# Optimization experiments

Hardware: AMD Instinct MI355X
Metric: run time of the kernel (lower is better)

The kernel has to match this reference:

```python
import jax, jax.numpy as jnp
import numpy as np

B, H, W = 2, 64, 1024
C1, C2 = 64, 128
MLP = [128, 128]
KH, KW = 5, 5
NS = 3
DIST = 100.0
BN_EPS = 1e-5


def setup_inputs() -> dict:
    key = jax.random.key(0)
    ks = jax.random.split(key, 12)
    inp = {
        "xyz1_proj": jax.random.normal(ks[0], (B, H, W, 3), jnp.float32),
        "xyz2_proj": jax.random.normal(ks[1], (B, H, W, 3), jnp.float32),
        "feat1_proj": jax.random.normal(ks[2], (B, H, W, C1), jnp.float32),
        "feat2_proj": jax.random.normal(ks[3], (B, H, W, C2), jnp.float32),
    }
    cin = C1 + C2
    chans = [cin] + MLP
    for i in range(len(MLP)):
        inp[f"w{i}"] = jax.random.normal(ks[4 + 2 * i], (chans[i], chans[i + 1]), jnp.float32) * 0.05
        inp[f"b{i}"] = jnp.zeros((chans[i + 1],), jnp.float32)
        inp[f"g{i}"] = jnp.ones((chans[i + 1],), jnp.float32)
        inp[f"be{i}"] = jnp.zeros((chans[i + 1],), jnp.float32)
    return inp


def _grid_knn(xyz1, xyz2):
    """Structured-grid KNN (no_sort_knn): for each query pixel, scan a KHxKW
    window in row-major order and take the first NS in-bounds neighbors whose
    squared distance is below DIST^2. Returns flat neighbor indices (B,N,NS)
    and a validity mask (B,N,NS,1)."""
    b, h, w, _ = xyz1.shape
    n = h * w
    k = KH * KW
    x1 = xyz1.reshape(b, n, 3)
    x2 = xyz2.reshape(b, n, 3)
    oh = jnp.repeat(jnp.arange(KH) - KH // 2, KW)   # (K,)
    ow = jnp.tile(jnp.arange(KW) - KW // 2, KH)     # (K,)
    nh = jnp.arange(h)[:, None, None] + oh[None, None, :]   # (H,1,K)
    nw = jnp.arange(w)[None, :, None] + ow[None, None, :]   # (1,W,K)
    inb = ((nh >= 0) & (nh < h)) & ((nw >= 0) & (nw < w))    # (H,W,K)
    flat = jnp.clip(nh, 0, h - 1) * w + jnp.clip(nw, 0, w - 1)
    flat = jnp.broadcast_to(flat, (h, w, k)).reshape(n, k)
    inb = jnp.broadcast_to(inb, (h, w, k)).reshape(n, k)
    # window gather: (B,N,K,3)
    neigh = jnp.take(x2, flat.reshape(-1), axis=1).reshape(b, n, k, 3)
    sq = jnp.sum(jnp.square(neigh - x1[:, :, None, :]), -1)  # (B,N,K)
    valid = inb[None] & (sq < DIST * DIST)
    v = valid.astype(jnp.int32)
    rank = jnp.cumsum(v, -1) - v  # rank among valid, scan order
    sel, fnd = [], []
    for j in range(NS):
        hit = valid & (rank == j)
        sel.append(jnp.argmax(hit, -1))
        fnd.append(jnp.any(hit, -1))
    sel = jnp.stack(sel, -1)          # (B,N,NS) window slot
    found = jnp.stack(fnd, -1)        # (B,N,NS)
    flat_b = jnp.broadcast_to(flat[None], (b, n, k))
    sel_flat = jnp.take_along_axis(flat_b, sel, axis=-1)
    sel_flat = jnp.where(found, sel_flat, 0)  # zeros like the init buffers
    mask = found.astype(x1.dtype)[..., None]  # (B,N,NS,1)
    return sel_flat, mask


def _gather(feat_flat, sel_flat):
    # feat_flat: (B,N,C), sel_flat: (B,N,NS) -> (B,N,NS,C)
    b, n, c = feat_flat.shape
    idx = sel_flat.reshape(b, n * NS, 1)
    g = jnp.take_along_axis(feat_flat, jnp.broadcast_to(idx, (b, n * NS, c)), axis=1)
    return g.reshape(b, n, NS, c)


def reference(xyz1_proj, xyz2_proj, feat1_proj, feat2_proj,
              w0, b0, g0, be0, w1, b1, g1, be1):
    b, h, w, _ = xyz1_proj.shape
    n = h * w
    xyz1 = xyz1_proj.reshape(b, n, 3)
    xyz2 = xyz2_proj.reshape(b, n, 3)
    feat2 = feat2_proj.reshape(b, n, -1)

    sel_flat, mask = _grid_knn(xyz1_proj, xyz2_proj)
    mask = jax.lax.stop_gradient(mask)

    grouped_xyz = _gather(xyz2, sel_flat) * mask          # (B,N,NS,3)
    grouped_feat = _gather(feat2, sel_flat) * mask        # (B,N,NS,C2)

    dist = jnp.sum(jnp.square(grouped_xyz - xyz1[:, :, None, :]), -1)  # (B,N,NS)
    dist = jnp.where(dist < 1e-10, jnp.full_like(dist, 1e-10), dist)
    norm = jnp.sum(1.0 / dist, axis=2, keepdims=True)     # (B,N,1)
    weight = (1.0 / dist) / norm                          # (B,N,NS)
    interp = jnp.sum(grouped_feat * weight[..., None], axis=2)  # (B,N,C2)

    x = jnp.concatenate([feat1_proj.reshape(b, n, -1), interp], -1)  # (B,N,C1+C2)

    # 1x1 conv MLP with training-mode BatchNorm + ReLU
    for (wi, bi, gi, bei) in ((w0, b0, g0, be0), (w1, b1, g1, be1)):
        x = x @ wi + bi
        mu = jnp.mean(x, axis=(0, 1))
        var = jnp.var(x, axis=(0, 1))
        x = (x - mu) * jax.lax.rsqrt(var + BN_EPS) * gi + bei
        x = jax.nn.relu(x)
    return x  # (B, H*W, MLP[-1])
```

## Files before the change

### kernel.cpp

```cpp
#include <hip/hip_runtime.h>

#define H_    64
#define W_    1024
#define NPT   65536
#define NTOT  131072
#define C1_   64
#define C2_   128
#define CIN_  192
#define CM_   128
#define NS_   3
#define DIST2_ 10000.0f
#define BN_EPS_ 1e-5f
#define NSLOT 32
#define XP    132

typedef __attribute__((ext_vector_type(8))) short short8;
typedef __attribute__((ext_vector_type(4))) float floatx4;

static __device__ __forceinline__ unsigned short f2bf(float f) {
    unsigned int u = __float_as_uint(f);
    u += 0x7fffu + ((u >> 16) & 1u);
    return (unsigned short)(u >> 16);
}
static __device__ __forceinline__ float bflo(unsigned u) { return __uint_as_float(u << 16); }
static __device__ __forceinline__ float bfhi(unsigned u) { return __uint_as_float(u & 0xffff0000u); }
static __device__ __forceinline__ unsigned packbf(float a, float b) {
    return (unsigned)f2bf(a) | ((unsigned)f2bf(b) << 16);
}

__global__ __launch_bounds__(256) void prep_w_kernel(
    const float* __restrict__ w0, const float* __restrict__ w1,
    unsigned short* __restrict__ w0F, unsigned short* __restrict__ w1F)
{
    int tid = blockIdx.x * 256 + threadIdx.x;
    if (tid < 3072) {
        int c = tid, lane = c & 63, nt = (c >> 6) & 7, kk = c >> 9;
        int n = nt * 16 + (lane & 15);
        int kb = kk * 32 + (lane >> 4) * 8;
        #pragma unroll
        for (int j = 0; j < 8; j++)
            w0F[(size_t)c * 8 + j] = f2bf(w0[(size_t)(kb + j) * CM_ + n]);
    } else if (tid < 5120) {
        int c = tid - 3072, lane = c & 63, nt = (c >> 6) & 7, kk = c >> 9;
        int n = nt * 16 + (lane & 15);
        int kb = kk * 32 + (lane >> 4) * 8;
        #pragma unroll
        for (int j = 0; j < 8; j++)
            w1F[(size_t)c * 8 + j] = f2bf(w1[(size_t)(kb + j) * CM_ + n]);
    }
}

static __device__ __forceinline__ void bn_finish_lds(
    const float* __restrict__ slots, const float* __restrict__ g,
    const float* __restrict__ be, float* bnpL, int t)
{
    if (t < CM_) {
        float s = 0.f, q2 = 0.f;
        #pragma unroll
        for (int sl = 0; sl < NSLOT; sl++) {
            s  += slots[sl * 256 + t];
            q2 += slots[sl * 256 + CM_ + t];
        }
        const float invn = 1.0f / (float)NTOT;
        float mu = s * invn, var = q2 * invn - mu * mu;
        float sc = g[t] * rsqrtf(var + BN_EPS_);
        bnpL[t] = sc;
        bnpL[CM_ + t] = be[t] - mu * sc;
    }
}

__global__ __launch_bounds__(256, 2) void fused1_kernel(
    const float* __restrict__ xyz1, const float* __restrict__ xyz2,
    const float* __restrict__ feat1, const float* __restrict__ feat2,
    const unsigned short* __restrict__ w0F, const float* __restrict__ b0,
    uint4* __restrict__ y0w4, float* __restrict__ slots0)
{
    __shared__ __align__(16) char smem[64 * XP * 2];
    __shared__ int   selL[64][NS_];
    __shared__ float wgtL[64][NS_];
    __shared__ float wsum[4][CM_], wsq[4][CM_];

    float (*sqL)[28] = (float (*)[28])smem;
    unsigned short (*xstage)[XP] = (unsigned short (*)[XP])smem;

    const int t = threadIdx.x;
    const int blk = blockIdx.x;
    const int pbase = blk * 64;
    const int bidx = blk >> 10;
    const int wv = t >> 6, lane = t & 63;
    const int m = lane & 15, q = lane >> 4;
    const int lr = wv * 16 + m;
    const int row0 = pbase + lr;

    short8 af[2];
    #pragma unroll
    for (int kk = 0; kk < 2; kk++) {
        const float* sp = feat1 + (size_t)row0 * C1_ + kk * 32 + q * 8;
        float4 fa = *(const float4*)(sp), fb = *(const float4*)(sp + 4);
        short8 a;
        a[0] = f2bf(fa.x); a[1] = f2bf(fa.y); a[2] = f2bf(fa.z); a[3] = f2bf(fa.w);
        a[4] = f2bf(fb.x); a[5] = f2bf(fb.y); a[6] = f2bf(fb.z); a[7] = f2bf(fb.w);
        af[kk] = a;
    }

    {
        const int p = t >> 2, g = t & 3;
        const int pt = pbase + p;
        const int n = pt & (NPT - 1);
        const int h = n >> 10, w = n & (W_ - 1);
        const float* p1 = xyz1 + (size_t)pt * 3;
        float x1 = p1[0], y1 = p1[1], z1 = p1[2];
        const float* x2b = xyz2 + (size_t)bidx * NPT * 3;
        #pragma unroll
        for (int j = 0; j < 7; j++) {
            int k = g * 7 + j;
            if (k < 25) {
                int dh = k / 5 - 2, dw = k % 5 - 2;
                int nh = h + dh, nw = w + dw;
                bool inb = (nh >= 0) && (nh < H_) && (nw >= 0) && (nw < W_);
                int ch = min(max(nh, 0), H_ - 1);
                int cw = min(max(nw, 0), W_ - 1);
                const float* p2 = x2b + (size_t)(ch * W_ + cw) * 3;
                float dx = p2[0] - x1, dy = p2[1] - y1, dz = p2[2] - z1;
                sqL[p][k] = inb ? (dx * dx + dy * dy + dz * dz) : 3.4e38f;
            }
        }
    }
    __syncthreads();

    if (t < 64) {
        const int pt = pbase + t;
        const int n = pt & (NPT - 1);
        const int h = n >> 10, w = n & (W_ - 1);
        const float* p1 = xyz1 + (size_t)pt * 3;
        float x1 = p1[0], y1 = p1[1], z1 = p1[2];

        int   s0 = 0, s1 = 0, s2 = 0;
        float d0 = 0.f, d1 = 0.f, d2 = 0.f;
        int cnt = 0;
        #pragma unroll
        for (int k = 0; k < 25; k++) {
            const int dh = k / 5 - 2, dw = k % 5 - 2;
            int ch = min(max(h + dh, 0), H_ - 1);
            int cw = min(max(w + dw, 0), W_ - 1);
            int nidx = ch * W_ + cw;
            float sk = sqL[t][k];
            if (sk < DIST2_ && cnt < NS_) {
                if (cnt == 0)      { s0 = nidx; d0 = sk; }
                else if (cnt == 1) { s1 = nidx; d1 = sk; }
                else               { s2 = nidx; d2 = sk; }
                cnt++;
            }
        }
        float self2 = x1 * x1 + y1 * y1 + z1 * z1;
        float dd0 = (cnt > 0) ? d0 : self2;
        float dd1 = (cnt > 1) ? d1 : self2;
        float dd2 = (cnt > 2) ? d2 : self2;
        dd0 = fmaxf(dd0, 1e-10f); dd1 = fmaxf(dd1, 1e-10f); dd2 = fmaxf(dd2, 1e-10f);
        float i0 = 1.0f / dd0, i1 = 1.0f / dd1, i2 = 1.0f / dd2;
        float norm = i0 + i1 + i2;
        selL[t][0] = (cnt > 0) ? s0 : 0;
        selL[t][1] = (cnt > 1) ? s1 : 0;
        selL[t][2] = (cnt > 2) ? s2 : 0;
        wgtL[t][0] = (cnt > 0) ? i0 / norm : 0.f;
        wgtL[t][1] = (cnt > 1) ? i1 / norm : 0.f;
        wgtL[t][2] = (cnt > 2) ? i2 / norm : 0.f;
    }
    __syncthreads();

    const float* f2b = feat2 + (size_t)bidx * NPT * C2_;
    #pragma unroll
    for (int i = 0; i < 8; i++) {
        int idx = t + i * 256;
        int p = idx >> 5, c4 = (idx & 31) << 2;
        float ax = 0.f, ay = 0.f, az = 0.f, aw = 0.f;
        #pragma unroll
        for (int j = 0; j < NS_; j++) {
            float wj = wgtL[p][j];
            const float4 f = *(const float4*)(f2b + (size_t)selL[p][j] * C2_ + c4);
            ax += wj * f.x; ay += wj * f.y; az += wj * f.z; aw += wj * f.w;
        }
        ushort4 u;
        u.x = f2bf(ax); u.y = f2bf(ay); u.z = f2bf(az); u.w = f2bf(aw);
        *(ushort4*)&xstage[p][c4] = u;
    }
    __syncthreads();

    floatx4 acc[8];
    #pragma unroll
    for (int nt = 0; nt < 8; nt++) acc[nt] = (floatx4){0.f, 0.f, 0.f, 0.f};

    #pragma unroll
    for (int kk = 0; kk < 6; kk++) {
        short8 bw[8];
        #pragma unroll
        for (int nt = 0; nt < 8; nt++)
            bw[nt] = *(const short8*)(w0F + ((size_t)(kk * 8 + nt) * 64 + lane) * 8);
        short8 a = (kk < 2) ? af[kk]
                            : *(const short8*)&xstage[lr][(kk - 2) * 32 + q * 8];
        #pragma unroll
        for (int nt = 0; nt < 8; nt++)
            acc[nt] = __builtin_amdgcn_mfma_f32_16x16x32_bf16(a, bw[nt], acc[nt], 0, 0, 0);
    }

    #pragma unroll
    for (int nt2 = 0; nt2 < 4; nt2++) {
        const int ntA = 2 * nt2, ntB = ntA + 1;
        const int nA = ntA * 16 + m, nB = ntB * 16 + m;
        float bvA = b0[nA], bvB = b0[nB];
        unsigned u0 = packbf(acc[ntA][0] + bvA, acc[ntA][1] + bvA);
        unsigned u1 = packbf(acc[ntA][2] + bvA, acc[ntA][3] + bvA);
        unsigned u2 = packbf(acc[ntB][0] + bvB, acc[ntB][1] + bvB);
        unsigned u3 = packbf(acc[ntB][2] + bvB, acc[ntB][3] + bvB);
        y0w4[((size_t)(blk * 4 + wv) * 4 + nt2) * 64 + lane] = make_uint4(u0, u1, u2, u3);
        float a0 = bflo(u0), a1 = bfhi(u0), a2 = bflo(u1), a3 = bfhi(u1);
        float b0v = bflo(u2), b1v = bfhi(u2), b2v = bflo(u3), b3v = bfhi(u3);
        float sA = a0 + a1 + a2 + a3, qA = a0*a0 + a1*a1 + a2*a2 + a3*a3;
        float sB = b0v + b1v + b2v + b3v, qB = b0v*b0v + b1v*b1v + b2v*b2v + b3v*b3v;
        sA += __shfl_xor(sA, 16, 64); qA += __shfl_xor(qA, 16, 64);
        sA += __shfl_xor(sA, 32, 64); qA += __shfl_xor(qA, 32, 64);
        sB += __shfl_xor(sB, 16, 64); qB += __shfl_xor(qB, 16, 64);
        sB += __shfl_xor(sB, 32, 64); qB += __shfl_xor(qB, 32, 64);
        if (q == 0) {
            wsum[wv][nA] = sA; wsq[wv][nA] = qA;
            wsum[wv][nB] = sB; wsq[wv][nB] = qB;
        }
    }
    __syncthreads();

    float* slot = slots0 + (size_t)(blk & (NSLOT - 1)) * 256;
    if (t < CM_)
        atomicAdd(&slot[t], wsum[0][t] + wsum[1][t] + wsum[2][t] + wsum[3][t]);
    else
        atomicAdd(&slot[t], wsq[0][t - CM_] + wsq[1][t - CM_] + wsq[2][t - CM_] + wsq[3][t - CM_]);
}

__global__ __launch_bounds__(256, 2) void fused2_kernel(
    const uint4* __restrict__ y0w4, const float* __restrict__ slots0,
    const float* __restrict__ g0, const float* __restrict__ be0,
    const unsigned short* __restrict__ w1F, const float* __restrict__ b1,
    uint4* __restrict__ y1w4, float* __restrict__ slots1)
{
    __shared__ unsigned short x1s[64][XP];
    __shared__ float wsum[4][CM_], wsq[4][CM_];
    __shared__ float bnpL[2 * CM_];

    const int t = threadIdx.x;
    const int blk = blockIdx.x;
    const int wv = t >> 6, lane = t & 63;
    const int m = lane & 15, q = lane >> 4;
    const int lr = wv * 16 + m;

    short8 bw0[8];
    #pragma unroll
    for (int nt = 0; nt < 8; nt++)
        bw0[nt] = *(const short8*)(w1F + ((size_t)nt * 64 + lane) * 8);

    bn_finish_lds(slots0, g0, be0, bnpL, t);
    __syncthreads();

    #pragma unroll
    for (int nt2 = 0; nt2 < 4; nt2++) {
        const int nA = (2 * nt2) * 16 + m, nB = nA + 16;
        float scA = bnpL[nA], shA = bnpL[CM_ + nA];
        float scB = bnpL[nB], shB = bnpL[CM_ + nB];
        uint4 u = y0w4[((size_t)(blk * 4 + wv) * 4 + nt2) * 64 + lane];
        int rb = wv * 16 + q * 4;
        x1s[rb + 0][nA] = f2bf(fmaxf(bflo(u.x) * scA + shA, 0.f));
        x1s[rb + 1][nA] = f2bf(fmaxf(bfhi(u.x) * scA + shA, 0.f));
        x1s[rb + 2][nA] = f2bf(fmaxf(bflo(u.y) * scA + shA, 0.f));
        x1s[rb + 3][nA] = f2bf(fmaxf(bfhi(u.y) * scA + shA, 0.f));
        x1s[rb + 0][nB] = f2bf(fmaxf(bflo(u.z) * scB + shB, 0.f));
        x1s[rb + 1][nB] = f2bf(fmaxf(bfhi(u.z) * scB + shB, 0.f));
        x1s[rb + 2][nB] = f2bf(fmaxf(bflo(u.w) * scB + shB, 0.f));
        x1s[rb + 3][nB] = f2bf(fmaxf(bfhi(u.w) * scB + shB, 0.f));
    }
    __syncthreads();

    floatx4 acc[8];
    #pragma unroll
    for (int nt = 0; nt < 8; nt++) acc[nt] = (floatx4){0.f, 0.f, 0.f, 0.f};

    #pragma unroll
    for (int kk = 0; kk < 4; kk++) {
        short8 bw[8];
        #pragma unroll
        for (int nt = 0; nt < 8; nt++)
            bw[nt] = (kk == 0) ? bw0[nt]
                   : *(const short8*)(w1F + ((size_t)(kk * 8 + nt) * 64 + lane) * 8);
        short8 a = *(const short8*)&x1s[lr][kk * 32 + q * 8];
        #pragma unroll
        for (int nt = 0; nt < 8; nt++)
            acc[nt] = __builtin_amdgcn_mfma_f32_16x16x32_bf16(a, bw[nt], acc[nt], 0, 0, 0);
    }

    #pragma unroll
    for (int nt2 = 0; nt2 < 4; nt2++) {
        const int ntA = 2 * nt2, ntB = ntA + 1;
        const int nA = ntA * 16 + m, nB = ntB * 16 + m;
        float bvA = b1[nA], bvB = b1[nB];
        unsigned u0 = packbf(acc[ntA][0] + bvA, acc[ntA][1] + bvA);
        unsigned u1 = packbf(acc[ntA][2] + bvA, acc[ntA][3] + bvA);
        unsigned u2 = packbf(acc[ntB][0] + bvB, acc[ntB][1] + bvB);
        unsigned u3 = packbf(acc[ntB][2] + bvB, acc[ntB][3] + bvB);
        y1w4[((size_t)(blk * 4 + wv) * 4 + nt2) * 64 + lane] = make_uint4(u0, u1, u2, u3);
        float a0 = bflo(u0), a1 = bfhi(u0), a2 = bflo(u1), a3 = bfhi(u1);
        float c0 = bflo(u2), c1 = bfhi(u2), c2 = bflo(u3), c3 = bfhi(u3);
        float sA = a0 + a1 + a2 + a3, qA = a0*a0 + a1*a1 + a2*a2 + a3*a3;
        float sB = c0 + c1 + c2 + c3, qB = c0*c0 + c1*c1 + c2*c2 + c3*c3;
        sA += __shfl_xor(sA, 16, 64); qA += __shfl_xor(qA, 16, 64);
        sA += __shfl_xor(sA, 32, 64); qA += __shfl_xor(qA, 32, 64);
        sB += __shfl_xor(sB, 16, 64); qB += __shfl_xor(qB, 16, 64);
        sB += __shfl_xor(sB, 32, 64); qB += __shfl_xor(qB, 32, 64);
        if (q == 0) {
            wsum[wv][nA] = sA; wsq[wv][nA] = qA;
            wsum[wv][nB] = sB; wsq[wv][nB] = qB;
        }
    }
    __syncthreads();

    float* slot = slots1 + (size_t)(blk & (NSLOT - 1)) * 256;
    if (t < CM_)
        atomicAdd(&slot[t], wsum[0][t] + wsum[1][t] + wsum[2][t] + wsum[3][t]);
    else
        atomicAdd(&slot[t], wsq[0][t - CM_] + wsq[1][t - CM_] + wsq[2][t - CM_] + wsq[3][t - CM_]);
}

__global__ __launch_bounds__(256) void bn_out_kernel(
    const uint4* __restrict__ y1w4, const float* __restrict__ slots1,
    const float* __restrict__ g1, const float* __restrict__ be1,
    float* __restrict__ out)
{
    __shared__ float xo[64][XP];
    __shared__ float bnpL[2 * CM_];
    const int t = threadIdx.x;
    const int blk = blockIdx.x;
    const int wv = t >> 6, lane = t & 63;
    const int m = lane & 15, q = lane >> 4;

    bn_finish_lds(slots1, g1, be1, bnpL, t);
    __syncthreads();

    #pragma unroll
    for (int nt2 = 0; nt2 < 4; nt2++) {
        const int nA = (2 * nt2) * 16 + m, nB = nA + 16;
        float scA = bnpL[nA], shA = bnpL[CM_ + nA];
        float scB = bnpL[nB], shB = bnpL[CM_ + nB];
        uint4 u = y1w4[((size_t)(blk * 4 + wv) * 4 + nt2) * 64 + lane];
        int rb = wv * 16 + q * 4;
        xo[rb + 0][nA] = fmaxf(bflo(u.x) * scA + shA, 0.f);
        xo[rb + 1][nA] = fmaxf(bfhi(u.x) * scA + shA, 0.f);
        xo[rb + 2][nA] = fmaxf(bflo(u.y) * scA + shA, 0.f);
        xo[rb + 3][nA] = fmaxf(bfhi(u.y) * scA + shA, 0.f);
        xo[rb + 0][nB] = fmaxf(bflo(u.z) * scB + shB, 0.f);
        xo[rb + 1][nB] = fmaxf(bfhi(u.z) * scB + shB, 0.f);
        xo[rb + 2][nB] = fmaxf(bflo(u.w) * scB + shB, 0.f);
        xo[rb + 3][nB] = fmaxf(bfhi(u.w) * scB + shB, 0.f);
    }
    __syncthreads();

    const int pbase = blk * 64;
    #pragma unroll
    for (int i = 0; i < 8; i++) {
        int idx = t + i * 256;
        int p = idx >> 5, c4 = (idx & 31) << 2;
        float4 v = *(const float4*)&xo[p][c4];
        *(float4*)(out + (size_t)(pbase + p) * CM_ + c4) = v;
    }
}

extern "C" void kernel_launch(void* const* d_in, const int* in_sizes, int n_in,
                              void* d_out, int out_size, void* d_ws, size_t ws_size,
                              hipStream_t stream)
{
    const float* xyz1  = (const float*)d_in[0];
    const float* xyz2  = (const float*)d_in[1];
    const float* feat1 = (const float*)d_in[2];
    const float* feat2 = (const float*)d_in[3];
    const float* w0    = (const float*)d_in[4];
    const float* b0    = (const float*)d_in[5];
    const float* g0    = (const float*)d_in[6];
    const float* be0   = (const float*)d_in[7];
    const float* w1    = (const float*)d_in[8];
    const float* b1    = (const float*)d_in[9];
    const float* g1    = (const float*)d_in[10];
    const float* be1   = (const float*)d_in[11];
    float* out = (float*)d_out;

    char* ws = (char*)d_ws;
    float* slots0       = (float*)(ws);
    float* slots1       = (float*)(ws + (size_t)NSLOT * 256 * 4);
    char*  p            = ws + 2 * (size_t)NSLOT * 256 * 4;
    unsigned short* w0F = (unsigned short*)p;  p += (size_t)CIN_ * CM_ * 2;
    unsigned short* w1F = (unsigned short*)p;  p += (size_t)CM_ * CM_ * 2;
    uint4* y0w4         = (uint4*)p;           p += (size_t)NTOT * CM_ * 2;
    uint4* y1w4         = (uint4*)p;

    hipMemsetAsync(ws, 0, 2 * (size_t)NSLOT * 256 * 4, stream);

    prep_w_kernel<<<20, 256, 0, stream>>>(w0, w1, w0F, w1F);
    fused1_kernel<<<NTOT / 64, 256, 0, stream>>>(xyz1, xyz2, feat1, feat2,
                                                 w0F, b0, y0w4, slots0);
    fused2_kernel<<<NTOT / 64, 256, 0, stream>>>(y0w4, slots0, g0, be0,
                                                 w1F, b1, y1w4, slots1);
    bn_out_kernel<<<NTOT / 64, 256, 0, stream>>>(y1w4, slots1, g1, be1, out);
}
```

Measured before the change: 224.9 us.

## Recompute second GEMM in output kernel instead of storing intermediate activations

The second layer's kernel now only accumulates BatchNorm statistics and no longer writes its bf16 pre-activation output. A new final kernel re-reads the first layer's output, reapplies BN0+ReLU, recomputes the second matmul, and applies BN1+ReLU before writing the result. This removes one full write and one full read of the intermediate buffer at the cost of an extra read of the first-layer output and a duplicated MFMA GEMM.

```diff
diff --git a/kernel.cpp b/kernel.cpp
--- a/kernel.cpp
+++ b/kernel.cpp
@@ -235,11 +235,11 @@
         atomicAdd(&slot[t], wsq[0][t - CM_] + wsq[1][t - CM_] + wsq[2][t - CM_] + wsq[3][t - CM_]);
 }
 
-__global__ __launch_bounds__(256, 2) void fused2_kernel(
+__global__ __launch_bounds__(256, 2) void fused2s_kernel(
     const uint4* __restrict__ y0w4, const float* __restrict__ slots0,
     const float* __restrict__ g0, const float* __restrict__ be0,
     const unsigned short* __restrict__ w1F, const float* __restrict__ b1,
-    uint4* __restrict__ y1w4, float* __restrict__ slots1)
+    float* __restrict__ slots1)
 {
     __shared__ unsigned short x1s[64][XP];
     __shared__ float wsum[4][CM_], wsq[4][CM_];
@@ -303,7 +303,6 @@
         unsigned u1 = packbf(acc[ntA][2] + bvA, acc[ntA][3] + bvA);
         unsigned u2 = packbf(acc[ntB][0] + bvB, acc[ntB][1] + bvB);
         unsigned u3 = packbf(acc[ntB][2] + bvB, acc[ntB][3] + bvB);
-        y1w4[((size_t)(blk * 4 + wv) * 4 + nt2) * 64 + lane] = make_uint4(u0, u1, u2, u3);
         float a0 = bflo(u0), a1 = bfhi(u0), a2 = bflo(u1), a3 = bfhi(u1);
         float c0 = bflo(u2), c1 = bfhi(u2), c2 = bflo(u3), c3 = bfhi(u3);
         float sA = a0 + a1 + a2 + a3, qA = a0*a0 + a1*a1 + a2*a2 + a3*a3;
@@ -326,36 +325,89 @@
         atomicAdd(&slot[t], wsq[0][t - CM_] + wsq[1][t - CM_] + wsq[2][t - CM_] + wsq[3][t - CM_]);
 }
 
-__global__ __launch_bounds__(256) void bn_out_kernel(
-    const uint4* __restrict__ y1w4, const float* __restrict__ slots1,
-    const float* __restrict__ g1, const float* __restrict__ be1,
-    float* __restrict__ out)
-{
-    __shared__ float xo[64][XP];
-    __shared__ float bnpL[2 * CM_];
+__global__ __launch_bounds__(256) void fused3_kernel(
+    const uint4* __restrict__ y0w4, const float* __restrict__ slots0,
+    const float* __restrict__ g0, const float* __restrict__ be0,
+    const unsigned short* __restrict__ w1F, const float* __restrict__ b1,
+    const float* __restrict__ slots1, const float* __restrict__ g1,
+    const float* __restrict__ be1, float* __restrict__ out)
+{
+    __shared__ __align__(16) char smem[64 * XP * 4];
+    __shared__ float bnp0L[2 * CM_], bnp1L[2 * CM_];
+    unsigned short (*x1s)[XP] = (unsigned short (*)[XP])smem;
+    float (*xo)[XP] = (float (*)[XP])smem;
+
     const int t = threadIdx.x;
     const int blk = blockIdx.x;
     const int wv = t >> 6, lane = t & 63;
     const int m = lane & 15, q = lane >> 4;
-
-    bn_finish_lds(slots1, g1, be1, bnpL, t);
+    const int lr = wv * 16 + m;
+
+    short8 bw0[8];
+    #pragma unroll
+    for (int nt = 0; nt < 8; nt++)
+        bw0[nt] = *(const short8*)(w1F + ((size_t)nt * 64 + lane) * 8);
+
+    bn_finish_lds(slots0, g0, be0, bnp0L, t);
+    bn_finish_lds(slots1, g1, be1, bnp1L, t);
     __syncthreads();
 
     #pragma unroll
     for (int nt2 = 0; nt2 < 4; nt2++) {
         const int nA = (2 * nt2) * 16 + m, nB = nA + 16;
-        float scA = bnpL[nA], shA = bnpL[CM_ + nA];
-        float scB = bnpL[nB], shB = bnpL[CM_ + nB];
-        uint4 u = y1w4[((size_t)(blk * 4 + wv) * 4 + nt2) * 64 + lane];
+        float scA = bnp0L[nA], shA = bnp0L[CM_ + nA];
+        float scB = bnp0L[nB], shB = bnp0L[CM_ + nB];
+        uint4 u = y0w4[((size_t)(blk * 4 + wv) * 4 + nt2) * 64 + lane];
         int rb = wv * 16 + q * 4;
-        xo[rb + 0][nA] = fmaxf(bflo(u.x) * scA + shA, 0.f);
-        xo[rb + 1][nA] = fmaxf(bfhi(u.x) * scA + shA, 0.f);
-        xo[rb + 2][nA] = fmaxf(bflo(u.y) * scA + shA, 0.f);
-        xo[rb + 3][nA] = fmaxf(bfhi(u.y) * scA + shA, 0.f);
-        xo[rb + 0][nB] = fmaxf(bflo(u.z) * scB + shB, 0.f);
-        xo[rb + 1][nB] = fmaxf(bfhi(u.z) * scB + shB, 0.f);
-        xo[rb + 2][nB] = fmaxf(bflo(u.w) * scB + shB, 0.f);
-        xo[rb + 3][nB] = fmaxf(bfhi(u.w) * scB + shB, 0.f);
+        x1s[rb + 0][nA] = f2bf(fmaxf(bflo(u.x) * scA + shA, 0.f));
+        x1s[rb + 1][nA] = f2bf(fmaxf(bfhi(u.x) * scA + shA, 0.f));
+        x1s[rb + 2][nA] = f2bf(fmaxf(bflo(u.y) * scA + shA, 0.f));
+        x1s[rb + 3][nA] = f2bf(fmaxf(bfhi(u.y) * scA + shA, 0.f));
+        x1s[rb + 0][nB] = f2bf(fmaxf(bflo(u.z) * scB + shB, 0.f));
+        x1s[rb + 1][nB] = f2bf(fmaxf(bfhi(u.z) * scB + shB, 0.f));
+        x1s[rb + 2][nB] = f2bf(fmaxf(bflo(u.w) * scB + shB, 0.f));
+        x1s[rb + 3][nB] = f2bf(fmaxf(bfhi(u.w) * scB + shB, 0.f));
+    }
+    __syncthreads();
+
+    floatx4 acc[8];
+    #pragma unroll
+    for (int nt = 0; nt < 8; nt++) acc[nt] = (floatx4){0.f, 0.f, 0.f, 0.f};
+
+    #pragma unroll
+    for (int kk = 0; kk < 4; kk++) {
+        short8 bw[8];
+        #pragma unroll
+        for (int nt = 0; nt < 8; nt++)
+            bw[nt] = (kk == 0) ? bw0[nt]
+                   : *(const short8*)(w1F + ((size_t)(kk * 8 + nt) * 64 + lane) * 8);
+        short8 a = *(const short8*)&x1s[lr][kk * 32 + q * 8];
+        #pragma unroll
+        for (int nt = 0; nt < 8; nt++)
+            acc[nt] = __builtin_amdgcn_mfma_f32_16x16x32_bf16(a, bw[nt], acc[nt], 0, 0, 0);
+    }
+    __syncthreads();
+
+    #pragma unroll
+    for (int nt2 = 0; nt2 < 4; nt2++) {
+        const int ntA = 2 * nt2, ntB = ntA + 1;
+        const int nA = ntA * 16 + m, nB = ntB * 16 + m;
+        float bvA = b1[nA], bvB = b1[nB];
+        unsigned u0 = packbf(acc[ntA][0] + bvA, acc[ntA][1] + bvA);
+        unsigned u1 = packbf(acc[ntA][2] + bvA, acc[ntA][3] + bvA);
+        unsigned u2 = packbf(acc[ntB][0] + bvB, acc[ntB][1] + bvB);
+        unsigned u3 = packbf(acc[ntB][2] + bvB, acc[ntB][3] + bvB);
+        float scA = bnp1L[nA], shA = bnp1L[CM_ + nA];
+        float scB = bnp1L[nB], shB = bnp1L[CM_ + nB];
+        int rb = wv * 16 + q * 4;
+        xo[rb + 0][nA] = fmaxf(bflo(u0) * scA + shA, 0.f);
+        xo[rb + 1][nA] = fmaxf(bfhi(u0) * scA + shA, 0.f);
+        xo[rb + 2][nA] = fmaxf(bflo(u1) * scA + shA, 0.f);
+        xo[rb + 3][nA] = fmaxf(bfhi(u1) * scA + shA, 0.f);
+        xo[rb + 0][nB] = fmaxf(bflo(u2) * scB + shB, 0.f);
+        xo[rb + 1][nB] = fmaxf(bfhi(u2) * scB + shB, 0.f);
+        xo[rb + 2][nB] = fmaxf(bflo(u3) * scB + shB, 0.f);
+        xo[rb + 3][nB] = fmaxf(bfhi(u3) * scB + shB, 0.f);
     }
     __syncthreads();
 
@@ -393,15 +445,15 @@
     char*  p            = ws + 2 * (size_t)NSLOT * 256 * 4;
     unsigned short* w0F = (unsigned short*)p;  p += (size_t)CIN_ * CM_ * 2;
     unsigned short* w1F = (unsigned short*)p;  p += (size_t)CM_ * CM_ * 2;
-    uint4* y0w4         = (uint4*)p;           p += (size_t)NTOT * CM_ * 2;
-    uint4* y1w4         = (uint4*)p;
+    uint4* y0w4         = (uint4*)p;
 
     hipMemsetAsync(ws, 0, 2 * (size_t)NSLOT * 256 * 4, stream);
 
     prep_w_kernel<<<20, 256, 0, stream>>>(w0, w1, w0F, w1F);
     fused1_kernel<<<NTOT / 64, 256, 0, stream>>>(xyz1, xyz2, feat1, feat2,
                                                  w0F, b0, y0w4, slots0);
-    fused2_kernel<<<NTOT / 64, 256, 0, stream>>>(y0w4, slots0, g0, be0,
-                                                 w1F, b1, y1w4, slots1);
-    bn_out_kernel<<<NTOT / 64, 256, 0, stream>>>(y1w4, slots1, g1, be1, out);
-}
+    fused2s_kernel<<<NTOT / 64, 256, 0, stream>>>(y0w4, slots0, g0, be0,
+                                                  w1F, b1, slots1);
+    fused3_kernel<<<NTOT / 64, 256, 0, stream>>>(y0w4, slots0, g0, be0,
+                                                 w1F, b1, slots1, g1, be1, out);
+}
```

Result: no change. 226.9 us (+0.9%).
